# Performance work log

Hardware: AMD Instinct MI355X
Metric: run time of the kernel (lower is better)

The kernel has to match this reference:

```python
import jax, jax.numpy as jnp
import numpy as np

G = 64  # fixed grid size hardcoded in the torch module

def setup_inputs() -> dict:
    key = jax.random.key(0)
    ks = jax.random.split(key, 12)
    N, H = 500000, 256
    s = lambda fan_in: 1.0 / np.sqrt(fan_in)
    return {
        "positions": jax.random.normal(ks[0], (N, 3), jnp.float32) * 2.0,
        "grid_points": jax.random.normal(ks[1], (G, 3), jnp.float32) * 2.0,
        "W1": jax.random.normal(ks[2], (3, 64), jnp.float32) * s(3),
        "b1": jnp.zeros((64,), jnp.float32),
        "W2": jax.random.normal(ks[3], (64, 128), jnp.float32) * s(64),
        "b2": jnp.zeros((128,), jnp.float32),
        "W3": jax.random.normal(ks[4], (128, H), jnp.float32) * s(128),
        "b3": jnp.zeros((H,), jnp.float32),
        "Wn1": jax.random.normal(ks[5], (H, H), jnp.float32) * s(H),
        "bn1": jnp.zeros((H,), jnp.float32),
        "Wn2": jax.random.normal(ks[6], (H, H), jnp.float32) * s(H),
        "bn2": jnp.zeros((H,), jnp.float32),
        "Wh1": jax.random.normal(ks[7], (4, H, 128), jnp.float32) * s(H),
        "bh1": jnp.zeros((4, 128), jnp.float32),
        "Wh2": jax.random.normal(ks[8], (4, 128, 1), jnp.float32) * s(128),
        "bh2": jnp.zeros((4, 1), jnp.float32),
    }

def reference(positions, grid_points, W1, b1, W2, b2, W3, b3,
              Wn1, bn1, Wn2, bn2, Wh1, bh1, Wh2, bh2):
    # crystal_encoder: per-atom MLP 3 -> 64 -> 128 -> 256 over ALL N atoms
    h = jax.nn.relu(positions @ W1 + b1)
    h = jax.nn.relu(h @ W2 + b2)
    feat = h @ W3 + b3                                   # [N, H]

    # _map_crystal_to_grid: only the first min(N, 64) atoms are mapped.
    pos64 = positions[:G]                                # [64, 3]
    d2 = jnp.sum((pos64[:, None, :] - grid_points[None, :, :]) ** 2, axis=-1)
    idx = jnp.argmin(d2, axis=-1)                        # [64] nearest grid point per atom
    winner = jnp.full((G,), -1, jnp.int32).at[idx].max(jnp.arange(G, dtype=jnp.int32))
    grid_feats = jnp.where(winner[:, None] >= 0,
                           feat[jnp.clip(winner, 0)], 0.0)  # [64, H]

    # TetrahedralAGINetwork (per-node MLP, channels-first output convention)
    x = grid_feats[None]                                 # [1, 64, H]
    y = jax.nn.relu(x @ Wn1 + bn1) @ Wn2 + bn2           # [1, 64, H]
    agg = jnp.mean(jnp.swapaxes(y, 1, 2), axis=-1)       # mean over nodes -> [1, H]

    # 4 property heads, batched: [4, 1, 1] -> [4] (order: band_gap,
    # elastic_modulus, thermal_conductivity, dielectric_constant)
    h1 = jax.nn.relu(jnp.einsum('bc,kcd->kbd', agg, Wh1) + bh1[:, None, :])
    props = jnp.einsum('kbd,kdo->kbo', h1, Wh2) + bh2[:, None, :]
    return props.reshape(4)
```

## Files before the change

### kernel.cpp

```cpp
#include <hip/hip_runtime.h>


__device__ __forceinline__ void async_cp16(const float* g, float* l) {
    __builtin_amdgcn_global_load_lds(
        (const __attribute__((address_space(1))) void*)g,
        (__attribute__((address_space(3))) void*)l, 16, 0, 0);
}
__device__ __forceinline__ void stage_contig(const float* g, float* l, int nfloats, int tid) {
    const int lane = tid & 63, wv = tid >> 6;
    const int ninst = nfloats >> 8;
    for (int i = wv; i < ninst; i += 4)
        async_cp16(g + i*256 + lane*4, l + i*256);
}
__device__ __forceinline__ void stage_slice32(const float* g, float* l, int ld, int j0, int nrows, int tid) {
    const int lane = tid & 63, wv = tid >> 6;
    const int r = lane >> 3, c4 = (lane & 7) << 2;
    const int ninst = nrows >> 3;
    for (int i = wv; i < ninst; i += 4)
        async_cp16(g + (i*8 + r)*ld + j0 + c4, l + i*256);
}

#define A_SMEM_BYTES (32768*4)

__global__ __launch_bounds__(256) void a_gf(
    const float* __restrict__ positions, const float* __restrict__ grid_pts,
    const float* __restrict__ W1, const float* __restrict__ b1,
    const float* __restrict__ W2, const float* __restrict__ b2,
    const float* __restrict__ W3, const float* __restrict__ b3,
    float* __restrict__ gf_ws)
{
    extern __shared__ float w3s[];
    __shared__ float pos_s[192], grid_s[192], w1_s[192], b1_s[64];
    __shared__ int   idx_s[64], win_s[8];
    __shared__ __align__(16) float h1s[8*64];
    __shared__ __align__(16) float h2s[8*128];

    const int tid = threadIdx.x;
    const int bg  = blockIdx.x;

    stage_contig(W3, w3s, 32768, tid);
    if (tid < 192) { pos_s[tid] = positions[tid]; grid_s[tid] = grid_pts[tid]; w1_s[tid] = W1[tid]; }
    if (tid >= 192) b1_s[tid - 192] = b1[tid - 192];
    const float bb2 = b2[tid & 127];
    const float bb3 = b3[tid];
    __syncthreads();

    if (tid < 64) {
        const float px = pos_s[tid*3], py = pos_s[tid*3+1], pz = pos_s[tid*3+2];
        float best = 3.4e38f; int bi = 0;
        for (int g = 0; g < 64; ++g) {
            const float dx = px - grid_s[g*3];
            const float dy = py - grid_s[g*3+1];
            const float dz = pz - grid_s[g*3+2];
            const float d2 = dx*dx + dy*dy + dz*dz;
            if (d2 < best) { best = d2; bi = g; }
        }
        idx_s[tid] = bi;
    }
    __syncthreads();
    if (tid < 8) {
        const int g = bg*8 + tid;
        int m = -1;
        for (int i = 0; i < 64; ++i) if (idx_s[i] == g) m = i;
        win_s[tid] = m;
    }
    __syncthreads();

    #pragma unroll
    for (int u = 0; u < 2; ++u) {
        const int e  = tid + u*256;
        const int lr = e >> 6, k = e & 63;
        int r = win_s[lr]; if (r < 0) r = 0;
        const float acc = b1_s[k] + pos_s[r*3]*w1_s[k] + pos_s[r*3+1]*w1_s[64+k]
                                  + pos_s[r*3+2]*w1_s[128+k];
        h1s[lr*64 + k] = fmaxf(acc, 0.f);
    }
    __syncthreads();

    {
        const int d = tid & 127, t0 = tid >> 7;
        float acc[4];
        #pragma unroll
        for (int m = 0; m < 4; ++m) acc[m] = bb2;
        for (int kc = 0; kc < 64; kc += 16) {
            float w[16];
            #pragma unroll
            for (int u = 0; u < 16; ++u) w[u] = W2[(kc+u)*128 + d];
            #pragma unroll
            for (int u = 0; u < 16; u += 4) {
                #pragma unroll
                for (int m = 0; m < 4; ++m) {
                    const float4 h4 = *(const float4*)&h1s[(t0 + 2*m)*64 + kc + u];
                    acc[m] += h4.x*w[u] + h4.y*w[u+1] + h4.z*w[u+2] + h4.w*w[u+3];
                }
            }
        }
        #pragma unroll
        for (int m = 0; m < 4; ++m)
            h2s[(t0 + 2*m)*128 + d] = fmaxf(acc[m], 0.f);
    }
    __syncthreads();

    {
        const int j = tid;
        float ag[8];
        #pragma unroll
        for (int t = 0; t < 8; ++t) ag[t] = 0.f;
        for (int dc = 0; dc < 128; dc += 16) {
            float w[16];
            #pragma unroll
            for (int u = 0; u < 16; ++u) w[u] = w3s[(dc+u)*256 + j];
            #pragma unroll
            for (int u = 0; u < 16; u += 4) {
                #pragma unroll
                for (int t = 0; t < 8; ++t) {
                    const float4 h4 = *(const float4*)&h2s[t*128 + dc + u];
                    ag[t] += h4.x*w[u] + h4.y*w[u+1] + h4.z*w[u+2] + h4.w*w[u+3];
                }
            }
        }
        #pragma unroll
        for (int t = 0; t < 8; ++t)
            gf_ws[(bg*8 + t)*256 + j] = (win_s[t] >= 0) ? (ag[t] + bb3) : 0.f;
    }
}

__global__ __launch_bounds__(256) void k2_tpart(
    const float* __restrict__ Wn1, const float* __restrict__ bn1,
    const float* __restrict__ gf_ws, float* __restrict__ tpart_ws)
{
    __shared__ __align__(16) float wn1_s[256*32];
    __shared__ __align__(16) float gf_s[8*256];
    __shared__ float r_s[256];

    const int tid = threadIdx.x;
    const int bg  = blockIdx.x >> 3;
    const int j0  = (blockIdx.x & 7) * 32;
    stage_slice32(Wn1, wn1_s, 256, j0, 256, tid);
    stage_contig(gf_ws + bg*8*256, gf_s, 8*256, tid);

    const int jl = tid & 31, t = tid >> 5;
    const float bb = bn1[j0 + jl];
    __syncthreads();

    float acc = bb;
    for (int cc = 0; cc < 256; cc += 32) {
        float w[32];
        #pragma unroll
        for (int u = 0; u < 32; ++u) w[u] = wn1_s[(cc+u)*32 + jl];
        #pragma unroll
        for (int u = 0; u < 32; u += 4) {
            const float4 g4 = *(const float4*)&gf_s[t*256 + cc + u];
            acc += g4.x*w[u] + g4.y*w[u+1] + g4.z*w[u+2] + g4.w*w[u+3];
        }
    }
    r_s[tid] = fmaxf(acc, 0.f);
    __syncthreads();
    if (t == 0) {
        float ps = 0.f;
        #pragma unroll
        for (int tt = 0; tt < 8; ++tt) ps += r_s[tt*32 + jl];
        tpart_ws[bg*256 + j0 + jl] = ps;
    }
}

#define CD_SMEM_BYTES (32768*4)

__global__ __launch_bounds__(256) void cd_head(
    const float* __restrict__ Wn2, const float* __restrict__ bn2,
    const float* __restrict__ Wh1, const float* __restrict__ bh1,
    const float* __restrict__ Wh2, const float* __restrict__ bh2,
    const float* __restrict__ tpart_ws,
    float* __restrict__ out)
{
    extern __shared__ float sm[];
    __shared__ __align__(16) float tp_s[2048];
    __shared__ __align__(16) float tbar_s[256];
    __shared__ __align__(16) float agg_s[256];
    __shared__ __align__(16) float h1h_s[128];
    __shared__ __align__(16) float wh2_s[128];

    float* bufA = sm;
    float* bufB = sm + 16384;

    const int tid = threadIdx.x;
    const int k   = blockIdx.x;

    stage_contig(tpart_ws, tp_s, 2048, tid);
    stage_contig(Wn2,          bufA, 16384, tid);
    stage_contig(Wn2 + 16384,  bufB, 16384, tid);
    const float bbn2  = bn2[tid];
    const float bbh1k = (tid < 128) ? bh1[k*128 + tid] : 0.f;
    if (tid < 128) wh2_s[tid] = Wh2[k*128 + tid];
    const float bbh2k = bh2[k];
    __syncthreads();

    {
        float tb = 0.f;
        #pragma unroll
        for (int q = 0; q < 8; ++q) tb += tp_s[q*256 + tid];
        tbar_s[tid] = tb * (1.f/64.f);
    }
    __syncthreads();

    float acc = bbn2;
    for (int jc = 0; jc < 64; jc += 32) {
        float w[32];
        #pragma unroll
        for (int u = 0; u < 32; ++u) w[u] = bufA[(jc+u)*256 + tid];
        #pragma unroll
        for (int u = 0; u < 32; u += 4) {
            const float4 t4 = *(const float4*)&tbar_s[jc + u];
            acc += t4.x*w[u] + t4.y*w[u+1] + t4.z*w[u+2] + t4.w*w[u+3];
        }
    }
    __syncthreads();
    stage_contig(Wn2 + 32768, bufA, 16384, tid);
    for (int jc = 64; jc < 128; jc += 32) {
        float w[32];
        #pragma unroll
        for (int u = 0; u < 32; ++u) w[u] = bufB[(jc-64+u)*256 + tid];
        #pragma unroll
        for (int u = 0; u < 32; u += 4) {
            const float4 t4 = *(const float4*)&tbar_s[jc + u];
            acc += t4.x*w[u] + t4.y*w[u+1] + t4.z*w[u+2] + t4.w*w[u+3];
        }
    }
    __syncthreads();
    stage_contig(Wn2 + 49152, bufB, 16384, tid);
    for (int jc = 128; jc < 192; jc += 32) {
        float w[32];
        #pragma unroll
        for (int u = 0; u < 32; ++u) w[u] = bufA[(jc-128+u)*256 + tid];
        #pragma unroll
        for (int u = 0; u < 32; u += 4) {
            const float4 t4 = *(const float4*)&tbar_s[jc + u];
            acc += t4.x*w[u] + t4.y*w[u+1] + t4.z*w[u+2] + t4.w*w[u+3];
        }
    }
    __syncthreads();
    for (int jc = 192; jc < 256; jc += 32) {
        float w[32];
        #pragma unroll
        for (int u = 0; u < 32; ++u) w[u] = bufB[(jc-192+u)*256 + tid];
        #pragma unroll
        for (int u = 0; u < 32; u += 4) {
            const float4 t4 = *(const float4*)&tbar_s[jc + u];
            acc += t4.x*w[u] + t4.y*w[u+1] + t4.z*w[u+2] + t4.w*w[u+3];
        }
    }
    agg_s[tid] = acc;
    __syncthreads();
    stage_contig(Wh1 + k*32768,         bufA, 16384, tid);
    stage_contig(Wh1 + k*32768 + 16384, bufB, 16384, tid);
    __syncthreads();

    if (tid < 128) {
        const int d = tid;
        float a = bbh1k;
        for (int cc = 0; cc < 128; cc += 16) {
            float wa[16];
            #pragma unroll
            for (int u = 0; u < 16; ++u) wa[u] = bufA[(cc+u)*128 + d];
            #pragma unroll
            for (int u = 0; u < 16; u += 4) {
                const float4 a4 = *(const float4*)&agg_s[cc + u];
                a += a4.x*wa[u] + a4.y*wa[u+1] + a4.z*wa[u+2] + a4.w*wa[u+3];
            }
        }
        for (int cc = 128; cc < 256; cc += 16) {
            float wa[16];
            #pragma unroll
            for (int u = 0; u < 16; ++u) wa[u] = bufB[(cc-128+u)*128 + d];
            #pragma unroll
            for (int u = 0; u < 16; u += 4) {
                const float4 a4 = *(const float4*)&agg_s[cc + u];
                a += a4.x*wa[u] + a4.y*wa[u+1] + a4.z*wa[u+2] + a4.w*wa[u+3];
            }
        }
        h1h_s[d] = fmaxf(a, 0.f);
    }
    __syncthreads();
    if (tid == 0) {
        float a = bbh2k;
        for (int d = 0; d < 128; ++d) a += h1h_s[d] * wh2_s[d];
        out[k] = a;
    }
}

extern "C" void kernel_launch(void* const* d_in, const int* in_sizes, int n_in,
                              void* d_out, int out_size, void* d_ws, size_t ws_size,
                              hipStream_t stream) {
    const float* positions = (const float*)d_in[0];
    const float* grid      = (const float*)d_in[1];
    const float* W1  = (const float*)d_in[2];
    const float* b1  = (const float*)d_in[3];
    const float* W2  = (const float*)d_in[4];
    const float* b2  = (const float*)d_in[5];
    const float* W3  = (const float*)d_in[6];
    const float* b3  = (const float*)d_in[7];
    const float* Wn1 = (const float*)d_in[8];
    const float* bn1 = (const float*)d_in[9];
    const float* Wn2 = (const float*)d_in[10];
    const float* bn2 = (const float*)d_in[11];
    const float* Wh1 = (const float*)d_in[12];
    const float* bh1 = (const float*)d_in[13];
    const float* Wh2 = (const float*)d_in[14];
    const float* bh2 = (const float*)d_in[15];
    float* out = (float*)d_out;

    char* ws = (char*)d_ws;
    float* gf_ws    = (float*)(ws + 0);
    float* tpart_ws = (float*)(ws + 65536);

    (void)hipFuncSetAttribute((const void*)a_gf,
                              hipFuncAttributeMaxDynamicSharedMemorySize,
                              A_SMEM_BYTES);
    (void)hipFuncSetAttribute((const void*)cd_head,
                              hipFuncAttributeMaxDynamicSharedMemorySize,
                              CD_SMEM_BYTES);

    hipLaunchKernelGGL(a_gf,     dim3(8),  dim3(256), A_SMEM_BYTES, stream,
                       positions, grid, W1, b1, W2, b2, W3, b3, gf_ws);
    hipLaunchKernelGGL(k2_tpart, dim3(64), dim3(256), 0, stream,
                       Wn1, bn1, gf_ws, tpart_ws);
    hipLaunchKernelGGL(cd_head,  dim3(4),  dim3(256), CD_SMEM_BYTES, stream,
                       Wn2, bn2, Wh1, bh1, Wh2, bh2, tpart_ws, out);
}
```

Baseline: 109.5 us.

## Fuse grid-feature encoder and Wn1 partial kernel, recomputing features per block

The grid-feature encoder and the Wn1/ReLU partial-sum stage are merged into one kernel launched with 64 blocks. Each block recomputes the 8 grid features for its group straight into shared memory, then reuses the dynamic shared buffer to stage its Wn1 column slice. This removes one kernel launch and the global-memory round trip of the feature workspace. In exchange, the W3 staging and encoder compute are done 8 times redundantly, once per column-slice block.

Result: no change. 109.9 us (+0.4%).

```diff
diff --git a/kernel.cpp b/kernel.cpp
--- a/kernel.cpp
+++ b/kernel.cpp
@@ -20,25 +20,29 @@
         async_cp16(g + (i*8 + r)*ld + j0 + c4, l + i*256);
 }
 
-#define A_SMEM_BYTES (32768*4)
-
-__global__ __launch_bounds__(256) void a_gf(
+#define AB_SMEM_BYTES (32768*4)
+
+__global__ __launch_bounds__(256) void ab_fused(
     const float* __restrict__ positions, const float* __restrict__ grid_pts,
     const float* __restrict__ W1, const float* __restrict__ b1,
     const float* __restrict__ W2, const float* __restrict__ b2,
     const float* __restrict__ W3, const float* __restrict__ b3,
-    float* __restrict__ gf_ws)
+    const float* __restrict__ Wn1, const float* __restrict__ bn1,
+    float* __restrict__ tpart_ws)
 {
-    extern __shared__ float w3s[];
+    extern __shared__ float sm[];
     __shared__ float pos_s[192], grid_s[192], w1_s[192], b1_s[64];
     __shared__ int   idx_s[64], win_s[8];
     __shared__ __align__(16) float h1s[8*64];
     __shared__ __align__(16) float h2s[8*128];
+    __shared__ __align__(16) float gf_s[8*256];
+    __shared__ float r_s[256];
 
     const int tid = threadIdx.x;
-    const int bg  = blockIdx.x;
-
-    stage_contig(W3, w3s, 32768, tid);
+    const int blk = blockIdx.x;
+    const int bg  = blk >> 3;
+
+    stage_contig(W3, sm, 32768, tid);
     if (tid < 192) { pos_s[tid] = positions[tid]; grid_s[tid] = grid_pts[tid]; w1_s[tid] = W1[tid]; }
     if (tid >= 192) b1_s[tid - 192] = b1[tid - 192];
     const float bb2 = b2[tid & 127];
@@ -69,11 +73,11 @@
     #pragma unroll
     for (int u = 0; u < 2; ++u) {
         const int e  = tid + u*256;
-        const int lr = e >> 6, k = e & 63;
+        const int lr = e >> 6, kk = e & 63;
         int r = win_s[lr]; if (r < 0) r = 0;
-        const float acc = b1_s[k] + pos_s[r*3]*w1_s[k] + pos_s[r*3+1]*w1_s[64+k]
-                                  + pos_s[r*3+2]*w1_s[128+k];
-        h1s[lr*64 + k] = fmaxf(acc, 0.f);
+        const float acc = b1_s[kk] + pos_s[r*3]*w1_s[kk] + pos_s[r*3+1]*w1_s[64+kk]
+                                   + pos_s[r*3+2]*w1_s[128+kk];
+        h1s[lr*64 + kk] = fmaxf(acc, 0.f);
     }
     __syncthreads();
 
@@ -109,7 +113,7 @@
         for (int dc = 0; dc < 128; dc += 16) {
             float w[16];
             #pragma unroll
-            for (int u = 0; u < 16; ++u) w[u] = w3s[(dc+u)*256 + j];
+            for (int u = 0; u < 16; ++u) w[u] = sm[(dc+u)*256 + j];
             #pragma unroll
             for (int u = 0; u < 16; u += 4) {
                 #pragma unroll
@@ -121,46 +125,36 @@
         }
         #pragma unroll
         for (int t = 0; t < 8; ++t)
-            gf_ws[(bg*8 + t)*256 + j] = (win_s[t] >= 0) ? (ag[t] + bb3) : 0.f;
-    }
-}
-
-__global__ __launch_bounds__(256) void k2_tpart(
-    const float* __restrict__ Wn1, const float* __restrict__ bn1,
-    const float* __restrict__ gf_ws, float* __restrict__ tpart_ws)
-{
-    __shared__ __align__(16) float wn1_s[256*32];
-    __shared__ __align__(16) float gf_s[8*256];
-    __shared__ float r_s[256];
-
-    const int tid = threadIdx.x;
-    const int bg  = blockIdx.x >> 3;
-    const int j0  = (blockIdx.x & 7) * 32;
-    stage_slice32(Wn1, wn1_s, 256, j0, 256, tid);
-    stage_contig(gf_ws + bg*8*256, gf_s, 8*256, tid);
-
-    const int jl = tid & 31, t = tid >> 5;
-    const float bb = bn1[j0 + jl];
-    __syncthreads();
-
-    float acc = bb;
-    for (int cc = 0; cc < 256; cc += 32) {
-        float w[32];
-        #pragma unroll
-        for (int u = 0; u < 32; ++u) w[u] = wn1_s[(cc+u)*32 + jl];
-        #pragma unroll
-        for (int u = 0; u < 32; u += 4) {
-            const float4 g4 = *(const float4*)&gf_s[t*256 + cc + u];
-            acc += g4.x*w[u] + g4.y*w[u+1] + g4.z*w[u+2] + g4.w*w[u+3];
-        }
-    }
-    r_s[tid] = fmaxf(acc, 0.f);
-    __syncthreads();
-    if (t == 0) {
-        float ps = 0.f;
-        #pragma unroll
-        for (int tt = 0; tt < 8; ++tt) ps += r_s[tt*32 + jl];
-        tpart_ws[bg*256 + j0 + jl] = ps;
+            gf_s[t*256 + j] = (win_s[t] >= 0) ? (ag[t] + bb3) : 0.f;
+    }
+    __syncthreads();
+
+    {
+        const int j0 = (blk & 7) * 32;
+        stage_slice32(Wn1, sm, 256, j0, 256, tid);
+        const int jl = tid & 31, t = tid >> 5;
+        const float bb = bn1[j0 + jl];
+        __syncthreads();
+
+        float acc = bb;
+        for (int cc = 0; cc < 256; cc += 32) {
+            float w[32];
+            #pragma unroll
+            for (int u = 0; u < 32; ++u) w[u] = sm[(cc+u)*32 + jl];
+            #pragma unroll
+            for (int u = 0; u < 32; u += 4) {
+                const float4 g4 = *(const float4*)&gf_s[t*256 + cc + u];
+                acc += g4.x*w[u] + g4.y*w[u+1] + g4.z*w[u+2] + g4.w*w[u+3];
+            }
+        }
+        r_s[tid] = fmaxf(acc, 0.f);
+        __syncthreads();
+        if (t == 0) {
+            float ps = 0.f;
+            #pragma unroll
+            for (int tt = 0; tt < 8; ++tt) ps += r_s[tt*32 + jl];
+            tpart_ws[bg*256 + j0 + jl] = ps;
+        }
     }
 }
 
@@ -309,21 +303,17 @@
     const float* bh2 = (const float*)d_in[15];
     float* out = (float*)d_out;
 
-    char* ws = (char*)d_ws;
-    float* gf_ws    = (float*)(ws + 0);
-    float* tpart_ws = (float*)(ws + 65536);
-
-    (void)hipFuncSetAttribute((const void*)a_gf,
+    float* tpart_ws = (float*)d_ws;
+
+    (void)hipFuncSetAttribute((const void*)ab_fused,
                               hipFuncAttributeMaxDynamicSharedMemorySize,
-                              A_SMEM_BYTES);
+                              AB_SMEM_BYTES);
     (void)hipFuncSetAttribute((const void*)cd_head,
                               hipFuncAttributeMaxDynamicSharedMemorySize,
                               CD_SMEM_BYTES);
 
-    hipLaunchKernelGGL(a_gf,     dim3(8),  dim3(256), A_SMEM_BYTES, stream,
-                       positions, grid, W1, b1, W2, b2, W3, b3, gf_ws);
-    hipLaunchKernelGGL(k2_tpart, dim3(64), dim3(256), 0, stream,
-                       Wn1, bn1, gf_ws, tpart_ws);
+    hipLaunchKernelGGL(ab_fused, dim3(64), dim3(256), AB_SMEM_BYTES, stream,
+                       positions, grid, W1, b1, W2, b2, W3, b3, Wn1, bn1, tpart_ws);
     hipLaunchKernelGGL(cd_head,  dim3(4),  dim3(256), CD_SMEM_BYTES, stream,
                        Wn2, bn2, Wh1, bh1, Wh2, bh2, tpart_ws, out);
 }
```
